# Performance work log

Measured on AMD Instinct MI355X. Metric: run time of the kernel, lower is better.

The kernel has to match this reference:

```python
import jax, jax.numpy as jnp
import numpy as np

N_NODES = 100000
N_EDGES = 1200000
D = 64
EPS = 1e-12  # matches torch F.normalize eps


def l2norm(x):
    n = jnp.linalg.norm(x, axis=-1, keepdims=True)
    return x / jnp.maximum(n, EPS)


def sage_layer(x, src, dst, Wl, bl, Wr, scale):
    # mechanism.normalize: row-wise L2 normalize (noise_scale=0 -> perturb is identity)
    xn = l2norm(x)
    # agg = x_normalized + scatter-add of neighbor (source) features into targets
    agg = xn + jax.ops.segment_sum(xn[src], dst, num_segments=N_NODES)
    # MessageNorm(learn_scale=True): normalize(msg) * ||x||_2 * scale
    msg = l2norm(agg) * jnp.linalg.norm(x, axis=-1, keepdims=True) * scale
    # lin_l(msg) + lin_r(x)  (root_weight=True, lin_r has no bias)
    out = msg @ Wl.T + bl + x @ Wr.T
    return l2norm(out)


def setup_inputs() -> dict:
    key = jax.random.key(0)
    ks = jax.random.split(key, 7)
    s = 1.0 / np.sqrt(D)
    return {
        "x": jax.random.normal(ks[0], (N_NODES, D), jnp.float32),
        "Wl0": jax.random.normal(ks[1], (D, D), jnp.float32) * s,
        "bl0": jnp.zeros((D,), jnp.float32),
        "Wr0": jax.random.normal(ks[2], (D, D), jnp.float32) * s,
        "scale0": jnp.ones((), jnp.float32),
        "Wl1": jax.random.normal(ks[3], (D, D), jnp.float32) * s,
        "bl1": jnp.zeros((D,), jnp.float32),
        "Wr1": jax.random.normal(ks[4], (D, D), jnp.float32) * s,
        "scale1": jnp.ones((), jnp.float32),
        "edge_index": jax.random.randint(ks[5], (2, N_EDGES), 0, N_NODES, dtype=jnp.int32),
    }


def reference(x, Wl0, bl0, Wr0, scale0, Wl1, bl1, Wr1, scale1, edge_index):
    src, dst = edge_index[0], edge_index[1]
    h = sage_layer(x, src, dst, Wl0, bl0, Wr0, scale0)
    h = jax.nn.relu(h)  # activation after layer 0 (not pred layer); dropout=identity (eval)
    h = sage_layer(h, src, dst, Wl1, bl1, Wr1, scale1)
    return h  # last layer of pred module: no bn/dropout/activation
```

## Files before the change

kernel.cpp:

```cpp
#include <hip/hip_runtime.h>

#define D 64
#define EPS 1e-12f
#define WPITCH 68
#define BSHIFT 8
#define BW 256
#define NBMAX 2048
#define NBLK 256

typedef unsigned short u16;

__device__ __forceinline__ float bf2f(u16 u) {
    return __uint_as_float(((unsigned)u) << 16);
}
__device__ __forceinline__ u16 f2bf(float f) {
    unsigned u = __float_as_uint(f);
    u += 0x7fffu + ((u >> 16) & 1u);
    return (u16)(u >> 16);
}
__device__ __forceinline__ float loadf(const void* p, size_t i, int bf) {
    return bf ? bf2f(((const u16*)p)[i]) : ((const float*)p)[i];
}

#define FMA4(acc, s, v)                       \
    do {                                      \
        acc.x = fmaf((s), (v).x, acc.x);      \
        acc.y = fmaf((s), (v).y, acc.y);      \
        acc.z = fmaf((s), (v).z, acc.z);      \
        acc.w = fmaf((s), (v).w, acc.w);      \
    } while (0)

__global__ __launch_bounds__(64) void detect_kernel(const u16* __restrict__ x,
                                                    int* __restrict__ flag) {
    int lane = threadIdx.x;
    int bad = 0;
    for (int i = 0; i < 64; ++i) {
        u16 u = x[lane * 64 + i];
        int e = (u >> 7) & 0xFF;
        if (e >= 0xC0) bad = 1;
    }
    unsigned long long b = __ballot(bad);
    if (lane == 0) *flag = (b == 0ull) ? 1 : 0;
}


__global__ __launch_bounds__(256) void zero_kernel(int* __restrict__ a, int n) {
    int i = blockIdx.x * blockDim.x + threadIdx.x;
    if (i < n) a[i] = 0;
}

__global__ __launch_bounds__(256) void bhist_kernel(const int* __restrict__ dst,
                                                    int* __restrict__ blockhist,
                                                    int E, int NB) {
    __shared__ int lh[NBMAX];
    const int b = blockIdx.x, t = threadIdx.x;
    const int per = (E + NBLK - 1) / NBLK;
    const int e0 = b * per, e1 = min(E, e0 + per);
    if (NB <= NBMAX) {
        for (int i = t; i < NB; i += 256) lh[i] = 0;
        __syncthreads();
        for (int e = e0 + t; e < e1; e += 256)
            atomicAdd(&lh[dst[e] >> BSHIFT], 1);
        __syncthreads();
        for (int i = t; i < NB; i += 256) blockhist[i * NBLK + b] = lh[i];
    } else {
        for (int e = e0 + t; e < e1; e += 256)
            atomicAdd(&blockhist[(dst[e] >> BSHIFT) * NBLK + b], 1);
    }
}

__global__ __launch_bounds__(256) void scanA_kernel(const int* __restrict__ a,
                                                    int* __restrict__ partials, int M) {
    int b = blockIdx.x, t = threadIdx.x;
    int base = b * 1024 + t * 4;
    int s = 0;
#pragma unroll
    for (int i = 0; i < 4; ++i) {
        int idx = base + i;
        if (idx < M) s += a[idx];
    }
    s += __shfl_xor(s, 32); s += __shfl_xor(s, 16); s += __shfl_xor(s, 8);
    s += __shfl_xor(s, 4);  s += __shfl_xor(s, 2);  s += __shfl_xor(s, 1);
    __shared__ int wt[4];
    if ((t & 63) == 0) wt[t >> 6] = s;
    __syncthreads();
    if (t == 0) partials[b] = wt[0] + wt[1] + wt[2] + wt[3];
}

__global__ __launch_bounds__(64) void scanB_kernel(int* __restrict__ partials, int NP) {
    int l = threadIdx.x;
    int total = 0;
    for (int base = 0; base < NP; base += 64) {
        int v = (base + l < NP) ? partials[base + l] : 0;
        int inc = v;
        for (int d = 1; d < 64; d <<= 1) {
            int u = __shfl_up(inc, d);
            if (l >= d) inc += u;
        }
        if (base + l < NP) partials[base + l] = inc - v + total;
        total += __shfl(inc, 63);
    }
}

__global__ __launch_bounds__(256) void scanC_kernel(const int* __restrict__ a,
                                                    const int* __restrict__ partials,
                                                    int* __restrict__ pos, int M) {
    int b = blockIdx.x, t = threadIdx.x;
    int base = b * 1024 + t * 4;
    int v[4];
    int s = 0;
#pragma unroll
    for (int i = 0; i < 4; ++i) {
        int idx = base + i;
        v[i] = (idx < M) ? a[idx] : 0;
        s += v[i];
    }
    int li = t & 63, w = t >> 6;
    int inc = s;
    for (int d = 1; d < 64; d <<= 1) {
        int u = __shfl_up(inc, d);
        if (li >= d) inc += u;
    }
    __shared__ int wt[4];
    if (li == 63) wt[w] = inc;
    __syncthreads();
    int woff = 0;
    for (int i = 0; i < w; ++i) woff += wt[i];
    int run = partials[b] + woff + (inc - s);
#pragma unroll
    for (int i = 0; i < 4; ++i) {
        int idx = base + i;
        if (idx < M) { pos[idx] = run; run += v[i]; }
    }
}

__global__ __launch_bounds__(256) void bmeta_kernel(const int* __restrict__ pos,
                                                    int* __restrict__ bcounts,
                                                    int* __restrict__ boffsets,
                                                    int NB, int E) {
    int i = blockIdx.x * blockDim.x + threadIdx.x;
    if (i < NB) {
        int s = pos[(size_t)i * NBLK];
        boffsets[i] = s;
        int nxt = (i + 1 < NB) ? pos[(size_t)(i + 1) * NBLK] : E;
        bcounts[i] = nxt - s;
    }
}

__global__ __launch_bounds__(256) void bfill_kernel(const int* __restrict__ src,
                                                    const int* __restrict__ dst,
                                                    int* __restrict__ pos,
                                                    int* __restrict__ bucket,
                                                    int E, int NB) {
    __shared__ int cur[NBMAX];
    const int b = blockIdx.x, t = threadIdx.x;
    const int per = (E + NBLK - 1) / NBLK;
    const int e0 = b * per, e1 = min(E, e0 + per);
    if (NB <= NBMAX) {
        for (int i = t; i < NB; i += 256) cur[i] = pos[(size_t)i * NBLK + b];
        __syncthreads();
        for (int e = e0 + t; e < e1; e += 256) {
            int s = src[e], d = dst[e];
            int p = atomicAdd(&cur[d >> BSHIFT], 1);
            bucket[p] = (s << BSHIFT) | (d & (BW - 1));
        }
    } else {
        for (int e = e0 + t; e < e1; e += 256) {
            int s = src[e], d = dst[e];
            int p = atomicAdd(&pos[(size_t)(d >> BSHIFT) * NBLK + b], 1);
            bucket[p] = (s << BSHIFT) | (d & (BW - 1));
        }
    }
}

__global__ __launch_bounds__(256) void csr_from_buckets_kernel(
    const int* __restrict__ bucket,
    const int* __restrict__ bcounts, const int* __restrict__ boffsets,
    int* __restrict__ counts, int* __restrict__ offsets,
    int* __restrict__ sorted_src, int N)
{
    __shared__ int hist[BW];
    __shared__ int cur[BW];
    __shared__ int wt[4];

    const int b = blockIdx.x;
    const int t = threadIdx.x;
    const int nbase = b << BSHIFT;
    const int ecnt = bcounts[b];
    const int ebase = boffsets[b];

    hist[t] = 0;
    __syncthreads();

    for (int e = t; e < ecnt; e += 256)
        atomicAdd(&hist[bucket[ebase + e] & (BW - 1)], 1);
    __syncthreads();

    int v = hist[t];
    int inc = v;
    for (int d = 1; d < 64; d <<= 1) {
        int u = __shfl_up(inc, d);
        if ((t & 63) >= d) inc += u;
    }
    if ((t & 63) == 63) wt[t >> 6] = inc;
    __syncthreads();
    int woff = 0;
    for (int i = 0; i < (t >> 6); ++i) woff += wt[i];
    int excl = inc - v + woff;
    cur[t] = excl;
    int node = nbase + t;
    if (node < N) {
        counts[node] = v;
        offsets[node] = ebase + excl;
    }
    __syncthreads();

    for (int e = t; e < ecnt; e += 256) {
        int pv = bucket[ebase + e];
        int p = atomicAdd(&cur[pv & (BW - 1)], 1);
        sorted_src[ebase + p] = ((unsigned)pv) >> BSHIFT;
    }
}


__global__ __launch_bounds__(256) void norm_init_kernel(
    const void* __restrict__ xin, float* __restrict__ nx, float* __restrict__ rnx,
    int N, const int* __restrict__ flagp)
{
    const int bf = *flagp;
    int node = (int)((blockIdx.x * blockDim.x + threadIdx.x) >> 6);
    int lane = threadIdx.x & 63;
    if (node >= N) return;
    float v = loadf(xin, (size_t)node * D + lane, bf);
    float s = v * v;
    s += __shfl_xor(s, 32); s += __shfl_xor(s, 16); s += __shfl_xor(s, 8);
    s += __shfl_xor(s, 4);  s += __shfl_xor(s, 2);  s += __shfl_xor(s, 1);
    if (lane == 0) {
        float n = sqrtf(s);
        nx[node] = n;
        rnx[node] = 1.0f / fmaxf(n, EPS);
    }
}

__device__ __forceinline__ float4 loadrow4(const void* p, int row, int lane16, int bf) {
    if (bf) {
        ushort4 u = ((const ushort4*)((const u16*)p + (size_t)row * D))[lane16];
        return make_float4(bf2f(u.x), bf2f(u.y), bf2f(u.z), bf2f(u.w));
    }
    return ((const float4*)((const float*)p + (size_t)row * D))[lane16];
}

__global__ __launch_bounds__(256) void gather_kernel(
    const int* __restrict__ offsets, const int* __restrict__ counts,
    const int* __restrict__ sorted_src,
    const void* __restrict__ xin, const float* __restrict__ rnx,
    float* __restrict__ agg, int N, const int* __restrict__ flagp)
{
    const int bf = *flagp;
    int node = (int)((blockIdx.x * blockDim.x + threadIdx.x) >> 6);
    int lane = threadIdx.x & 63;
    if (node >= N) return;
    const int lane16 = lane & 15, grp = lane >> 4;

    float4 acc = make_float4(0.f, 0.f, 0.f, 0.f);
    if (grp == 0) {
        float4 xs = loadrow4(xin, node, lane16, bf);
        FMA4(acc, rnx[node], xs);
    }

    const int start = offsets[node];
    const int deg = counts[node];
    for (int i = 0; i < deg; i += 64) {
        int cnt = min(deg - i, 64);
        int id = (lane < cnt) ? sorted_src[start + i + lane] : 0;
        int j = 0;
        for (; j + 8 <= cnt; j += 8) {
            int s0 = __shfl(id, j + grp);
            int s1 = __shfl(id, j + 4 + grp);
            float w0 = rnx[s0], w1 = rnx[s1];
            float4 v0 = loadrow4(xin, s0, lane16, bf);
            float4 v1 = loadrow4(xin, s1, lane16, bf);
            FMA4(acc, w0, v0);
            FMA4(acc, w1, v1);
        }
        if (j + 4 <= cnt) {
            int s0 = __shfl(id, j + grp);
            float w0 = rnx[s0];
            float4 v0 = loadrow4(xin, s0, lane16, bf);
            FMA4(acc, w0, v0);
            j += 4;
        }
        if (j < cnt) {
            int e = j + grp;
            int s0 = __shfl(id, min(e, cnt - 1));
            if (e < cnt) {
                float w0 = rnx[s0];
                float4 v0 = loadrow4(xin, s0, lane16, bf);
                FMA4(acc, w0, v0);
            }
        }
    }

    acc.x += __shfl_xor(acc.x, 16); acc.y += __shfl_xor(acc.y, 16);
    acc.z += __shfl_xor(acc.z, 16); acc.w += __shfl_xor(acc.w, 16);
    acc.x += __shfl_xor(acc.x, 32); acc.y += __shfl_xor(acc.y, 32);
    acc.z += __shfl_xor(acc.z, 32); acc.w += __shfl_xor(acc.w, 32);
    if (grp == 0)
        ((float4*)(agg + (size_t)node * D))[lane16] = acc;
}

#define KSTEP(kk, comp)                                                     \
    {                                                                       \
        float4 a = *((const float4*)(wlp + (kk) * WPITCH));                 \
        float4 b = *((const float4*)(wrp + (kk) * WPITCH));                 \
        FMA4(acc[0], m[0].comp, a); FMA4(acc[0], xf[0].comp, b);            \
        FMA4(acc[1], m[1].comp, a); FMA4(acc[1], xf[1].comp, b);            \
        FMA4(acc[2], m[2].comp, a); FMA4(acc[2], xf[2].comp, b);            \
        FMA4(acc[3], m[3].comp, a); FMA4(acc[3], xf[3].comp, b);            \
    }

__global__ __launch_bounds__(256) void epilogue_kernel(
    const float* __restrict__ agg, const float* __restrict__ nx,
    const void* __restrict__ xin,
    const void* __restrict__ wl, const void* __restrict__ bl,
    const void* __restrict__ wr, const void* __restrict__ scale_p,
    void* __restrict__ out, int N, const int* __restrict__ flagp, int relu)
{
    __shared__ float lds_wl[D * WPITCH];
    __shared__ float lds_wr[D * WPITCH];
    __shared__ float lds_bl[D];
    __shared__ float msgbuf[4][16 * WPITCH];

    const int bf = *flagp;
    const int t = threadIdx.x;
    for (int idx = t; idx < D * D; idx += 256) {
        int j = idx >> 6, k = idx & 63;
        lds_wl[k * WPITCH + j] = loadf(wl, idx, bf);
        lds_wr[k * WPITCH + j] = loadf(wr, idx, bf);
    }
    if (t < D) lds_bl[t] = loadf(bl, t, bf);
    __syncthreads();

    const float scl = loadf(scale_p, 0, bf);
    const int w = t >> 6, lane = t & 63;
    const int sub = lane >> 4, cg = lane & 15;

    const int node0 = blockIdx.x * 64 + w * 16 + sub * 4;
    int n[4];
    bool valid[4];
    float4 a4[4];
    float nxv[4];
#pragma unroll
    for (int r = 0; r < 4; ++r) {
        int nn = node0 + r;
        valid[r] = nn < N;
        n[r] = valid[r] ? nn : N - 1;
        a4[r] = ((const float4*)(agg + (size_t)n[r] * D))[cg];
        nxv[r] = nx[n[r]];
    }

    float* mrow = msgbuf[w];
#pragma unroll
    for (int r = 0; r < 4; ++r) {
        float4 v4 = a4[r];
        float s = v4.x * v4.x + v4.y * v4.y + v4.z * v4.z + v4.w * v4.w;
        s += __shfl_xor(s, 1); s += __shfl_xor(s, 2);
        s += __shfl_xor(s, 4); s += __shfl_xor(s, 8);
        float minv = scl * nxv[r] / fmaxf(sqrtf(s), EPS);
        *((float4*)(mrow + (sub * 4 + r) * WPITCH + cg * 4)) =
            make_float4(v4.x * minv, v4.y * minv, v4.z * minv, v4.w * minv);
    }

    float4 acc[4];
    {
        float4 b4 = ((const float4*)lds_bl)[cg];
#pragma unroll
        for (int r = 0; r < 4; ++r) acc[r] = b4;
    }

    const float* wlbase = lds_wl + cg * 4;
    const float* wrbase = lds_wr + cg * 4;

    if (bf) {
#pragma unroll
        for (int k4 = 0; k4 < 16; ++k4) {
            float4 m[4], xf[4];
#pragma unroll
            for (int r = 0; r < 4; ++r) {
                m[r] = *((const float4*)(mrow + (sub * 4 + r) * WPITCH + k4 * 4));
                ushort4 xu = ((const ushort4*)((const u16*)xin + (size_t)n[r] * D))[k4];
                xf[r] = make_float4(bf2f(xu.x), bf2f(xu.y), bf2f(xu.z), bf2f(xu.w));
            }
            const float* wlp = wlbase + (k4 * 4) * WPITCH;
            const float* wrp = wrbase + (k4 * 4) * WPITCH;
            KSTEP(0, x) KSTEP(1, y) KSTEP(2, z) KSTEP(3, w)
        }
    } else {
#pragma unroll
        for (int k4 = 0; k4 < 16; ++k4) {
            float4 m[4], xf[4];
#pragma unroll
            for (int r = 0; r < 4; ++r) {
                m[r] = *((const float4*)(mrow + (sub * 4 + r) * WPITCH + k4 * 4));
                xf[r] = ((const float4*)((const float*)xin + (size_t)n[r] * D))[k4];
            }
            const float* wlp = wlbase + (k4 * 4) * WPITCH;
            const float* wrp = wrbase + (k4 * 4) * WPITCH;
            KSTEP(0, x) KSTEP(1, y) KSTEP(2, z) KSTEP(3, w)
        }
    }

#pragma unroll
    for (int r = 0; r < 4; ++r) {
        float4 v = acc[r];
        float s2 = v.x * v.x + v.y * v.y + v.z * v.z + v.w * v.w;
        s2 += __shfl_xor(s2, 1); s2 += __shfl_xor(s2, 2);
        s2 += __shfl_xor(s2, 4); s2 += __shfl_xor(s2, 8);
        float inv = 1.0f / fmaxf(sqrtf(s2), EPS);
        float4 rv = make_float4(v.x * inv, v.y * inv, v.z * inv, v.w * inv);
        if (relu) {
            rv.x = fmaxf(rv.x, 0.f); rv.y = fmaxf(rv.y, 0.f);
            rv.z = fmaxf(rv.z, 0.f); rv.w = fmaxf(rv.w, 0.f);
        }
        if (valid[r]) {
            if (bf) {
                ushort4 o = make_ushort4(f2bf(rv.x), f2bf(rv.y), f2bf(rv.z), f2bf(rv.w));
                ((ushort4*)((u16*)out + (size_t)n[r] * D))[cg] = o;
            } else {
                ((float4*)((float*)out + (size_t)n[r] * D))[cg] = rv;
            }
        }
    }
}

extern "C" void kernel_launch(void* const* d_in, const int* in_sizes, int n_in,
                              void* d_out, int out_size, void* d_ws, size_t ws_size,
                              hipStream_t stream)
{
    const void* x   = d_in[0];
    const void* Wl0 = d_in[1];
    const void* bl0 = d_in[2];
    const void* Wr0 = d_in[3];
    const void* sc0 = d_in[4];
    const void* Wl1 = d_in[5];
    const void* bl1 = d_in[6];
    const void* Wr1 = d_in[7];
    const void* sc1 = d_in[8];
    const int* ei   = (const int*)d_in[9];

    const int N = in_sizes[0] / D;
    const int E = in_sizes[9] / 2;
    const int* src = ei;
    const int* dst = ei + E;

    const int NB = (N + BW - 1) >> BSHIFT;
    const int M  = NB * NBLK;
    const int NP = (M + 1023) / 1024;

    float* agg       = (float*)d_ws;
    float* nx        = agg + (size_t)N * D;
    float* rnx       = nx + N;
    int* flag        = (int*)(rnx + N);
    int* counts      = flag + 1;
    int* offsets     = counts + N;
    int* bcounts     = offsets + N;
    int* boffsets    = bcounts + NB;
    int* blockhist   = boffsets + NB;
    int* pos         = blockhist + M;
    int* partials    = pos + M;
    int* bucket      = partials + NP;
    int* sorted_src  = bucket + E;

    void* h = d_out;

    dim3 blk(256);
    int gridA  = (N + 3) / 4;
    int gridC  = (N + 63) / 64;

    detect_kernel<<<1, 64, 0, stream>>>((const u16*)x, flag);

    if (NB > NBMAX)
        zero_kernel<<<(M + 255) / 256, blk, 0, stream>>>(blockhist, M);
    bhist_kernel<<<NBLK, blk, 0, stream>>>(dst, blockhist, E, NB);
    scanA_kernel<<<NP, blk, 0, stream>>>(blockhist, partials, M);
    scanB_kernel<<<1, 64, 0, stream>>>(partials, NP);
    scanC_kernel<<<NP, blk, 0, stream>>>(blockhist, partials, pos, M);
    bmeta_kernel<<<(NB + 255) / 256, blk, 0, stream>>>(pos, bcounts, boffsets, NB, E);
    bfill_kernel<<<NBLK, blk, 0, stream>>>(src, dst, pos, bucket, E, NB);
    csr_from_buckets_kernel<<<NB, blk, 0, stream>>>(bucket, bcounts, boffsets,
                                                    counts, offsets, sorted_src, N);

    norm_init_kernel<<<gridA, blk, 0, stream>>>(x, nx, rnx, N, flag);
    gather_kernel<<<gridA, blk, 0, stream>>>(offsets, counts, sorted_src, x, rnx,
                                             agg, N, flag);
    epilogue_kernel<<<gridC, blk, 0, stream>>>(agg, nx, x, Wl0, bl0, Wr0, sc0,
                                               h, N, flag, 1);

    norm_init_kernel<<<gridA, blk, 0, stream>>>(h, nx, rnx, N, flag);
    gather_kernel<<<gridA, blk, 0, stream>>>(offsets, counts, sorted_src, h, rnx,
                                             agg, N, flag);
    epilogue_kernel<<<gridC, blk, 0, stream>>>(agg, nx, h, Wl1, bl1, Wr1, sc1,
                                               d_out, N, flag, 0);
}
```

Measured before the change: 368.1 us.

## Fuse second-layer norm into epilogue, shuffle edge weights, drop fp32 weight LDS staging

The first-layer epilogue now computes the row norm and reciprocal norm of its output and writes them directly. This removes the separate norm_init pass over h before the second gather. In the gather kernel, each lane loads rnx for its own source id once per 64-edge chunk, and the value is broadcast with shuffles instead of being loaded per edge. The epilogue keeps bf16 weights in LDS as u16 on the bf16 path. On the fp32 path it skips LDS staging and reads weights from global memory with strided scalar loads, which trades the staging cost for more global and cache traffic inside the inner loop.

```diff
diff --git a/kernel.cpp b/kernel.cpp
--- a/kernel.cpp
+++ b/kernel.cpp
@@ -3,6 +3,7 @@
 #define D 64
 #define EPS 1e-12f
 #define WPITCH 68
+#define WPU 68
 #define BSHIFT 8
 #define BW 256
 #define NBMAX 2048
@@ -20,6 +21,9 @@
 }
 __device__ __forceinline__ float loadf(const void* p, size_t i, int bf) {
     return bf ? bf2f(((const u16*)p)[i]) : ((const float*)p)[i];
+}
+__device__ __forceinline__ float4 cvt4(ushort4 u) {
+    return make_float4(bf2f(u.x), bf2f(u.y), bf2f(u.z), bf2f(u.w));
 }
 
 #define FMA4(acc, s, v)                       \
@@ -245,7 +249,7 @@
 __device__ __forceinline__ float4 loadrow4(const void* p, int row, int lane16, int bf) {
     if (bf) {
         ushort4 u = ((const ushort4*)((const u16*)p + (size_t)row * D))[lane16];
-        return make_float4(bf2f(u.x), bf2f(u.y), bf2f(u.z), bf2f(u.w));
+        return cvt4(u);
     }
     return ((const float4*)((const float*)p + (size_t)row * D))[lane16];
 }
@@ -273,11 +277,13 @@
     for (int i = 0; i < deg; i += 64) {
         int cnt = min(deg - i, 64);
         int id = (lane < cnt) ? sorted_src[start + i + lane] : 0;
+        float wvl = rnx[id];
         int j = 0;
         for (; j + 8 <= cnt; j += 8) {
             int s0 = __shfl(id, j + grp);
             int s1 = __shfl(id, j + 4 + grp);
-            float w0 = rnx[s0], w1 = rnx[s1];
+            float w0 = __shfl(wvl, j + grp);
+            float w1 = __shfl(wvl, j + 4 + grp);
             float4 v0 = loadrow4(xin, s0, lane16, bf);
             float4 v1 = loadrow4(xin, s1, lane16, bf);
             FMA4(acc, w0, v0);
@@ -285,7 +291,7 @@
         }
         if (j + 4 <= cnt) {
             int s0 = __shfl(id, j + grp);
-            float w0 = rnx[s0];
+            float w0 = __shfl(wvl, j + grp);
             float4 v0 = loadrow4(xin, s0, lane16, bf);
             FMA4(acc, w0, v0);
             j += 4;
@@ -293,8 +299,8 @@
         if (j < cnt) {
             int e = j + grp;
             int s0 = __shfl(id, min(e, cnt - 1));
+            float w0 = __shfl(wvl, min(e, cnt - 1));
             if (e < cnt) {
-                float w0 = rnx[s0];
                 float4 v0 = loadrow4(xin, s0, lane16, bf);
                 FMA4(acc, w0, v0);
             }
@@ -309,34 +315,54 @@
         ((float4*)(agg + (size_t)node * D))[lane16] = acc;
 }
 
-#define KSTEP(kk, comp)                                                     \
+#define KSTEP_BF(kk, comp)                                                  \
     {                                                                       \
-        float4 a = *((const float4*)(wlp + (kk) * WPITCH));                 \
-        float4 b = *((const float4*)(wrp + (kk) * WPITCH));                 \
+        float4 a = cvt4(*((const ushort4*)(wlpu + (kk) * WPU)));            \
+        float4 b = cvt4(*((const ushort4*)(wrpu + (kk) * WPU)));            \
         FMA4(acc[0], m[0].comp, a); FMA4(acc[0], xf[0].comp, b);            \
         FMA4(acc[1], m[1].comp, a); FMA4(acc[1], xf[1].comp, b);            \
         FMA4(acc[2], m[2].comp, a); FMA4(acc[2], xf[2].comp, b);            \
         FMA4(acc[3], m[3].comp, a); FMA4(acc[3], xf[3].comp, b);            \
     }
 
+#define KSTEP_F32(kk, comp)                                                 \
+    {                                                                       \
+        const int kabs_ = k4 * 4 + (kk);                                    \
+        float4 a = make_float4(wlg[(cg * 4 + 0) * D + kabs_],               \
+                               wlg[(cg * 4 + 1) * D + kabs_],               \
+                               wlg[(cg * 4 + 2) * D + kabs_],               \
+                               wlg[(cg * 4 + 3) * D + kabs_]);              \
+        float4 b = make_float4(wrg[(cg * 4 + 0) * D + kabs_],               \
+                               wrg[(cg * 4 + 1) * D + kabs_],               \
+                               wrg[(cg * 4 + 2) * D + kabs_],               \
+                               wrg[(cg * 4 + 3) * D + kabs_]);              \
+        FMA4(acc[0], m[0].comp, a); FMA4(acc[0], xf[0].comp, b);            \
+        FMA4(acc[1], m[1].comp, a); FMA4(acc[1], xf[1].comp, b);            \
+        FMA4(acc[2], m[2].comp, a); FMA4(acc[2], xf[2].comp, b);            \
+        FMA4(acc[3], m[3].comp, a); FMA4(acc[3], xf[3].comp, b);            \
+    }
+
 __global__ __launch_bounds__(256) void epilogue_kernel(
-    const float* __restrict__ agg, const float* __restrict__ nx,
-    const void* __restrict__ xin,
+    const float* __restrict__ agg, float* __restrict__ nx,
+    float* __restrict__ rnx, const void* __restrict__ xin,
     const void* __restrict__ wl, const void* __restrict__ bl,
     const void* __restrict__ wr, const void* __restrict__ scale_p,
-    void* __restrict__ out, int N, const int* __restrict__ flagp, int relu)
+    void* __restrict__ out, int N, const int* __restrict__ flagp,
+    int relu, int write_norm)
 {
-    __shared__ float lds_wl[D * WPITCH];
-    __shared__ float lds_wr[D * WPITCH];
+    __shared__ u16 lds_wlu[D * WPU];
+    __shared__ u16 lds_wru[D * WPU];
     __shared__ float lds_bl[D];
     __shared__ float msgbuf[4][16 * WPITCH];
 
     const int bf = *flagp;
     const int t = threadIdx.x;
-    for (int idx = t; idx < D * D; idx += 256) {
-        int j = idx >> 6, k = idx & 63;
-        lds_wl[k * WPITCH + j] = loadf(wl, idx, bf);
-        lds_wr[k * WPITCH + j] = loadf(wr, idx, bf);
+    if (bf) {
+        for (int idx = t; idx < D * D; idx += 256) {
+            int j = idx >> 6, k = idx & 63;
+            lds_wlu[k * WPU + j] = ((const u16*)wl)[idx];
+            lds_wru[k * WPU + j] = ((const u16*)wr)[idx];
+        }
     }
     if (t < D) lds_bl[t] = loadf(bl, t, bf);
     __syncthreads();
@@ -378,10 +404,9 @@
         for (int r = 0; r < 4; ++r) acc[r] = b4;
     }
 
-    const float* wlbase = lds_wl + cg * 4;
-    const float* wrbase = lds_wr + cg * 4;
-
     if (bf) {
+        const u16* wlb = lds_wlu + cg * 4;
+        const u16* wrb = lds_wru + cg * 4;
 #pragma unroll
         for (int k4 = 0; k4 < 16; ++k4) {
             float4 m[4], xf[4];
@@ -389,13 +414,15 @@
             for (int r = 0; r < 4; ++r) {
                 m[r] = *((const float4*)(mrow + (sub * 4 + r) * WPITCH + k4 * 4));
                 ushort4 xu = ((const ushort4*)((const u16*)xin + (size_t)n[r] * D))[k4];
-                xf[r] = make_float4(bf2f(xu.x), bf2f(xu.y), bf2f(xu.z), bf2f(xu.w));
+                xf[r] = cvt4(xu);
             }
-            const float* wlp = wlbase + (k4 * 4) * WPITCH;
-            const float* wrp = wrbase + (k4 * 4) * WPITCH;
-            KSTEP(0, x) KSTEP(1, y) KSTEP(2, z) KSTEP(3, w)
+            const u16* wlpu = wlb + (k4 * 4) * WPU;
+            const u16* wrpu = wrb + (k4 * 4) * WPU;
+            KSTEP_BF(0, x) KSTEP_BF(1, y) KSTEP_BF(2, z) KSTEP_BF(3, w)
         }
     } else {
+        const float* wlg = (const float*)wl;
+        const float* wrg = (const float*)wr;
 #pragma unroll
         for (int k4 = 0; k4 < 16; ++k4) {
             float4 m[4], xf[4];
@@ -404,9 +431,7 @@
                 m[r] = *((const float4*)(mrow + (sub * 4 + r) * WPITCH + k4 * 4));
                 xf[r] = ((const float4*)((const float*)xin + (size_t)n[r] * D))[k4];
             }
-            const float* wlp = wlbase + (k4 * 4) * WPITCH;
-            const float* wrp = wrbase + (k4 * 4) * WPITCH;
-            KSTEP(0, x) KSTEP(1, y) KSTEP(2, z) KSTEP(3, w)
+            KSTEP_F32(0, x) KSTEP_F32(1, y) KSTEP_F32(2, z) KSTEP_F32(3, w)
         }
     }
 
@@ -421,6 +446,16 @@
         if (relu) {
             rv.x = fmaxf(rv.x, 0.f); rv.y = fmaxf(rv.y, 0.f);
             rv.z = fmaxf(rv.z, 0.f); rv.w = fmaxf(rv.w, 0.f);
+        }
+        if (write_norm) {
+            float s3 = rv.x * rv.x + rv.y * rv.y + rv.z * rv.z + rv.w * rv.w;
+            s3 += __shfl_xor(s3, 1); s3 += __shfl_xor(s3, 2);
+            s3 += __shfl_xor(s3, 4); s3 += __shfl_xor(s3, 8);
+            if (valid[r] && cg == 0) {
+                float nn = sqrtf(s3);
+                nx[n[r]] = nn;
+                rnx[n[r]] = 1.0f / fmaxf(nn, EPS);
+            }
         }
         if (valid[r]) {
             if (bf) {
@@ -493,12 +528,11 @@
     norm_init_kernel<<<gridA, blk, 0, stream>>>(x, nx, rnx, N, flag);
     gather_kernel<<<gridA, blk, 0, stream>>>(offsets, counts, sorted_src, x, rnx,
                                              agg, N, flag);
-    epilogue_kernel<<<gridC, blk, 0, stream>>>(agg, nx, x, Wl0, bl0, Wr0, sc0,
-                                               h, N, flag, 1);
-
-    norm_init_kernel<<<gridA, blk, 0, stream>>>(h, nx, rnx, N, flag);
+    epilogue_kernel<<<gridC, blk, 0, stream>>>(agg, nx, rnx, x, Wl0, bl0, Wr0, sc0,
+                                               h, N, flag, 1, 1);
+
     gather_kernel<<<gridA, blk, 0, stream>>>(offsets, counts, sorted_src, h, rnx,
                                              agg, N, flag);
-    epilogue_kernel<<<gridC, blk, 0, stream>>>(agg, nx, h, Wl1, bl1, Wr1, sc1,
-                                               d_out, N, flag, 0);
-}
+    epilogue_kernel<<<gridC, blk, 0, stream>>>(agg, nx, rnx, h, Wl1, bl1, Wr1, sc1,
+                                               d_out, N, flag, 0, 0);
+}
```

Measured after the change: 529.6 us. +43.9%, slower.

## Fuse next-layer norm into epilogue, shuffle edge weights, prefetch rows

Applied to the files above, without the earlier changes.

The layer-0 epilogue now computes the row norms of its output and writes nx/rnx directly, removing the separate norm kernel before layer 1. In the gather, per-edge inverse norms are loaded once per lane with the edge ids and broadcast by shuffles, replacing dependent random loads. The epilogue also issues agg loads before weight staging and double-buffers the x row loads across the k loop. The fused norm is computed from unrounded values, which can differ slightly from the norm of the stored bf16 output.

```diff
diff --git a/kernel.cpp b/kernel.cpp
--- a/kernel.cpp
+++ b/kernel.cpp
@@ -20,6 +20,9 @@
 }
 __device__ __forceinline__ float loadf(const void* p, size_t i, int bf) {
     return bf ? bf2f(((const u16*)p)[i]) : ((const float*)p)[i];
+}
+__device__ __forceinline__ float4 cvt4(ushort4 u) {
+    return make_float4(bf2f(u.x), bf2f(u.y), bf2f(u.z), bf2f(u.w));
 }
 
 #define FMA4(acc, s, v)                       \
@@ -245,7 +248,7 @@
 __device__ __forceinline__ float4 loadrow4(const void* p, int row, int lane16, int bf) {
     if (bf) {
         ushort4 u = ((const ushort4*)((const u16*)p + (size_t)row * D))[lane16];
-        return make_float4(bf2f(u.x), bf2f(u.y), bf2f(u.z), bf2f(u.w));
+        return cvt4(u);
     }
     return ((const float4*)((const float*)p + (size_t)row * D))[lane16];
 }
@@ -273,11 +276,13 @@
     for (int i = 0; i < deg; i += 64) {
         int cnt = min(deg - i, 64);
         int id = (lane < cnt) ? sorted_src[start + i + lane] : 0;
+        float wvl = rnx[id];
         int j = 0;
         for (; j + 8 <= cnt; j += 8) {
             int s0 = __shfl(id, j + grp);
             int s1 = __shfl(id, j + 4 + grp);
-            float w0 = rnx[s0], w1 = rnx[s1];
+            float w0 = __shfl(wvl, j + grp);
+            float w1 = __shfl(wvl, j + 4 + grp);
             float4 v0 = loadrow4(xin, s0, lane16, bf);
             float4 v1 = loadrow4(xin, s1, lane16, bf);
             FMA4(acc, w0, v0);
@@ -285,7 +290,7 @@
         }
         if (j + 4 <= cnt) {
             int s0 = __shfl(id, j + grp);
-            float w0 = rnx[s0];
+            float w0 = __shfl(wvl, j + grp);
             float4 v0 = loadrow4(xin, s0, lane16, bf);
             FMA4(acc, w0, v0);
             j += 4;
@@ -293,8 +298,8 @@
         if (j < cnt) {
             int e = j + grp;
             int s0 = __shfl(id, min(e, cnt - 1));
+            float w0 = __shfl(wvl, min(e, cnt - 1));
             if (e < cnt) {
-                float w0 = rnx[s0];
                 float4 v0 = loadrow4(xin, s0, lane16, bf);
                 FMA4(acc, w0, v0);
             }
@@ -320,11 +325,12 @@
     }
 
 __global__ __launch_bounds__(256) void epilogue_kernel(
-    const float* __restrict__ agg, const float* __restrict__ nx,
-    const void* __restrict__ xin,
+    const float* __restrict__ agg, float* __restrict__ nx,
+    float* __restrict__ rnx, const void* __restrict__ xin,
     const void* __restrict__ wl, const void* __restrict__ bl,
     const void* __restrict__ wr, const void* __restrict__ scale_p,
-    void* __restrict__ out, int N, const int* __restrict__ flagp, int relu)
+    void* __restrict__ out, int N, const int* __restrict__ flagp,
+    int relu, int write_norm)
 {
     __shared__ float lds_wl[D * WPITCH];
     __shared__ float lds_wr[D * WPITCH];
@@ -333,6 +339,27 @@
 
     const int bf = *flagp;
     const int t = threadIdx.x;
+    const int w = t >> 6, lane = t & 63;
+    const int sub = lane >> 4, cg = lane & 15;
+
+    const int node0 = blockIdx.x * 64 + w * 16 + sub * 4;
+    int n[4];
+    bool valid[4];
+#pragma unroll
+    for (int r = 0; r < 4; ++r) {
+        int nn = node0 + r;
+        valid[r] = nn < N;
+        n[r] = valid[r] ? nn : N - 1;
+    }
+
+    float4 a4[4];
+    float nxv[4];
+#pragma unroll
+    for (int r = 0; r < 4; ++r) {
+        a4[r] = ((const float4*)(agg + (size_t)n[r] * D))[cg];
+        nxv[r] = nx[n[r]];
+    }
+
     for (int idx = t; idx < D * D; idx += 256) {
         int j = idx >> 6, k = idx & 63;
         lds_wl[k * WPITCH + j] = loadf(wl, idx, bf);
@@ -342,22 +369,6 @@
     __syncthreads();
 
     const float scl = loadf(scale_p, 0, bf);
-    const int w = t >> 6, lane = t & 63;
-    const int sub = lane >> 4, cg = lane & 15;
-
-    const int node0 = blockIdx.x * 64 + w * 16 + sub * 4;
-    int n[4];
-    bool valid[4];
-    float4 a4[4];
-    float nxv[4];
-#pragma unroll
-    for (int r = 0; r < 4; ++r) {
-        int nn = node0 + r;
-        valid[r] = nn < N;
-        n[r] = valid[r] ? nn : N - 1;
-        a4[r] = ((const float4*)(agg + (size_t)n[r] * D))[cg];
-        nxv[r] = nx[n[r]];
-    }
 
     float* mrow = msgbuf[w];
 #pragma unroll
@@ -382,31 +393,63 @@
     const float* wrbase = lds_wr + cg * 4;
 
     if (bf) {
+        const u16* xb[4];
+        ushort4 xu_cur[4];
+#pragma unroll
+        for (int r = 0; r < 4; ++r) {
+            xb[r] = (const u16*)xin + (size_t)n[r] * D;
+            xu_cur[r] = ((const ushort4*)xb[r])[0];
+        }
 #pragma unroll
         for (int k4 = 0; k4 < 16; ++k4) {
+            ushort4 xu_nxt[4];
+            if (k4 < 15) {
+#pragma unroll
+                for (int r = 0; r < 4; ++r)
+                    xu_nxt[r] = ((const ushort4*)xb[r])[k4 + 1];
+            }
             float4 m[4], xf[4];
 #pragma unroll
             for (int r = 0; r < 4; ++r) {
                 m[r] = *((const float4*)(mrow + (sub * 4 + r) * WPITCH + k4 * 4));
-                ushort4 xu = ((const ushort4*)((const u16*)xin + (size_t)n[r] * D))[k4];
-                xf[r] = make_float4(bf2f(xu.x), bf2f(xu.y), bf2f(xu.z), bf2f(xu.w));
+                xf[r] = cvt4(xu_cur[r]);
             }
             const float* wlp = wlbase + (k4 * 4) * WPITCH;
             const float* wrp = wrbase + (k4 * 4) * WPITCH;
             KSTEP(0, x) KSTEP(1, y) KSTEP(2, z) KSTEP(3, w)
+            if (k4 < 15) {
+#pragma unroll
+                for (int r = 0; r < 4; ++r) xu_cur[r] = xu_nxt[r];
+            }
         }
     } else {
+        const float* xb[4];
+        float4 xc[4];
+#pragma unroll
+        for (int r = 0; r < 4; ++r) {
+            xb[r] = (const float*)xin + (size_t)n[r] * D;
+            xc[r] = ((const float4*)xb[r])[0];
+        }
 #pragma unroll
         for (int k4 = 0; k4 < 16; ++k4) {
+            float4 xn_[4];
+            if (k4 < 15) {
+#pragma unroll
+                for (int r = 0; r < 4; ++r) xn_[r] = ((const float4*)xb[r])[k4 + 1];
+            }
             float4 m[4], xf[4];
 #pragma unroll
             for (int r = 0; r < 4; ++r) {
                 m[r] = *((const float4*)(mrow + (sub * 4 + r) * WPITCH + k4 * 4));
-                xf[r] = ((const float4*)((const float*)xin + (size_t)n[r] * D))[k4];
+                xf[r] = xc[r];
             }
             const float* wlp = wlbase + (k4 * 4) * WPITCH;
             const float* wrp = wrbase + (k4 * 4) * WPITCH;
             KSTEP(0, x) KSTEP(1, y) KSTEP(2, z) KSTEP(3, w)
+            if (k4 < 15) {
+#pragma unroll
+                for (int r = 0; r < 4; ++r) xc[r] = xn_[r];
+            }
         }
     }
 
@@ -421,6 +464,16 @@
         if (relu) {
             rv.x = fmaxf(rv.x, 0.f); rv.y = fmaxf(rv.y, 0.f);
             rv.z = fmaxf(rv.z, 0.f); rv.w = fmaxf(rv.w, 0.f);
+        }
+        if (write_norm) {
+            float s3 = rv.x * rv.x + rv.y * rv.y + rv.z * rv.z + rv.w * rv.w;
+            s3 += __shfl_xor(s3, 1); s3 += __shfl_xor(s3, 2);
+            s3 += __shfl_xor(s3, 4); s3 += __shfl_xor(s3, 8);
+            if (valid[r] && cg == 0) {
+                float nn = sqrtf(s3);
+                nx[n[r]] = nn;
+                rnx[n[r]] = 1.0f / fmaxf(nn, EPS);
+            }
         }
         if (valid[r]) {
             if (bf) {
@@ -493,12 +546,11 @@
     norm_init_kernel<<<gridA, blk, 0, stream>>>(x, nx, rnx, N, flag);
     gather_kernel<<<gridA, blk, 0, stream>>>(offsets, counts, sorted_src, x, rnx,
                                              agg, N, flag);
-    epilogue_kernel<<<gridC, blk, 0, stream>>>(agg, nx, x, Wl0, bl0, Wr0, sc0,
-                                               h, N, flag, 1);
-
-    norm_init_kernel<<<gridA, blk, 0, stream>>>(h, nx, rnx, N, flag);
+    epilogue_kernel<<<gridC, blk, 0, stream>>>(agg, nx, rnx, x, Wl0, bl0, Wr0, sc0,
+                                               h, N, flag, 1, 1);
+
     gather_kernel<<<gridA, blk, 0, stream>>>(offsets, counts, sorted_src, h, rnx,
                                              agg, N, flag);
-    epilogue_kernel<<<gridC, blk, 0, stream>>>(agg, nx, h, Wl1, bl1, Wr1, sc1,
-                                               d_out, N, flag, 0);
-}
+    epilogue_kernel<<<gridC, blk, 0, stream>>>(agg, nx, rnx, h, Wl1, bl1, Wr1, sc1,
+                                               d_out, N, flag, 0, 0);
+}
```

Result: slower. 443.7 us (+20.5%).
